# Kernel optimization log

Measured on AMD Instinct MI355X. Metric: run time of the kernel, lower is better.

The kernel has to match this reference:

```python
import jax, jax.numpy as jnp
from jax import lax
import numpy as np

EPS = 1e-6
DN = ('NCHW', 'OIHW', 'NCHW')  # conv dimension numbers matching torch F.conv2d


def setup_inputs() -> dict:
    key = jax.random.key(0)
    kx, ky = jax.random.split(key)
    B, C, H, W = 16, 3, 512, 512
    x = jax.random.normal(kx, (B, C, H, W), dtype=jnp.float32)
    y = jax.random.normal(ky, (B, C, H, W), dtype=jnp.float32)
    return {"x": x, "y": y}


def _box_smooth(v):
    # 7x7 uniform kernel repeated over 3 input channels -> 1 output channel,
    # every tap weighted 1/49 (matches kernel.repeat(1,3,1,1) in torch).
    k = jnp.full((1, v.shape[1], 7, 7), 1.0 / 49.0, dtype=v.dtype)
    return lax.conv_general_dilated(v, k, window_strides=(1, 1),
                                    padding=[(3, 3), (3, 3)],
                                    dimension_numbers=DN)


def reference(x, y):
    # conv is linear, so conv(x) - conv(y) == conv(x - y); avoids one conv pass
    diff = _box_smooth(x - y)           # [B, 1, H, W]
    return jnp.mean(jnp.sqrt(diff * diff + EPS))  # scalar Charbonnier loss
```

## Files before the change

### kernel.cpp

```cpp
#include <hip/hip_runtime.h>
#include <math.h>


namespace {
constexpr int kB = 16, kC = 3, kH = 512, kW = 512;
constexpr int ROWS = 2;
constexpr int INROWS = ROWS + 6;
constexpr int BANDS_PER_IMG = kH / ROWS;
constexpr int NBANDS = kB * BANDS_PER_IMG;
constexpr int WPB = 4;
constexpr int NT = WPB * 64;
constexpr int NB = NBANDS / WPB;
constexpr int NXCD = 8;
constexpr float EPS = 1e-6f;
}

struct RowRegs { float4 a[6]; float4 b[6]; };

__device__ __forceinline__ void issue_row(RowRegs& R,
                                          const float* __restrict__ xb,
                                          const float* __restrict__ yb,
                                          int rclamp, int c0) {
  const size_t HW = (size_t)kH * kW;
  const float* px = xb + (size_t)rclamp * kW + c0;
  const float* py = yb + (size_t)rclamp * kW + c0;
#pragma unroll
  for (int ch = 0; ch < 3; ++ch) {
    R.a[ch]     = *(const float4*)(px + ch * HW);
    R.b[ch]     = *(const float4*)(px + ch * HW + 4);
    R.a[3 + ch] = *(const float4*)(py + ch * HW);
    R.b[3 + ch] = *(const float4*)(py + ch * HW + 4);
  }
}

__global__ __launch_bounds__(NT, 1)
void charbox_kernel(const float* __restrict__ x, const float* __restrict__ y,
                    float* __restrict__ out) {
  __shared__ float red[WPB];

  const int tid  = threadIdx.x;
  const int lane = tid & 63;
  const int wid  = tid >> 6;
  const int swz  = (blockIdx.x % NXCD) * (NB / NXCD) + blockIdx.x / NXCD;
  const int band = swz * WPB + wid;
  const int b    = band >> 8;
  const int r0   = (band & 255) * ROWS;
  const size_t HW = (size_t)kH * kW;
  const float* xb = x + (size_t)b * kC * HW;
  const float* yb = y + (size_t)b * kC * HW;
  const int c0 = lane * 8;
  const int laneL = (lane + 63) & 63;
  const int laneR = (lane + 1) & 63;

  float v0[8], v1[8];
#pragma unroll
  for (int j = 0; j < 8; ++j) { v0[j] = 0.f; v1[j] = 0.f; }
  float acc = 0.f;

  RowRegs buf[2];
  issue_row(buf[0], xb, yb, max(r0 - 3, 0), c0);

#pragma unroll
  for (int it = 0; it < INROWS; ++it) {
    if (it + 1 < INROWS) {
      const int rn = r0 - 3 + it + 1;
      issue_row(buf[(it + 1) & 1], xb, yb, min(max(rn, 0), kH - 1), c0);
    }
    const RowRegs& R = buf[it & 1];
    const int r = r0 - 3 + it;
    const bool valid = (r >= 0) & (r < kH);

    float z[8];
    if (valid) {
      z[0] = (R.a[0].x - R.a[3].x) + (R.a[1].x - R.a[4].x) + (R.a[2].x - R.a[5].x);
      z[1] = (R.a[0].y - R.a[3].y) + (R.a[1].y - R.a[4].y) + (R.a[2].y - R.a[5].y);
      z[2] = (R.a[0].z - R.a[3].z) + (R.a[1].z - R.a[4].z) + (R.a[2].z - R.a[5].z);
      z[3] = (R.a[0].w - R.a[3].w) + (R.a[1].w - R.a[4].w) + (R.a[2].w - R.a[5].w);
      z[4] = (R.b[0].x - R.b[3].x) + (R.b[1].x - R.b[4].x) + (R.b[2].x - R.b[5].x);
      z[5] = (R.b[0].y - R.b[3].y) + (R.b[1].y - R.b[4].y) + (R.b[2].y - R.b[5].y);
      z[6] = (R.b[0].z - R.b[3].z) + (R.b[1].z - R.b[4].z) + (R.b[2].z - R.b[5].z);
      z[7] = (R.b[0].w - R.b[3].w) + (R.b[1].w - R.b[4].w) + (R.b[2].w - R.b[5].w);
    } else {
#pragma unroll
      for (int j = 0; j < 8; ++j) z[j] = 0.f;
    }

    const float l5 = __shfl(z[5], laneL, 64);
    const float l6 = __shfl(z[6], laneL, 64);
    const float l7 = __shfl(z[7], laneL, 64);
    const float g0 = __shfl(z[0], laneR, 64);
    const float g1 = __shfl(z[1], laneR, 64);
    const float g2 = __shfl(z[2], laneR, 64);
    float e[14];
    e[0] = lane ? l5 : 0.f;
    e[1] = lane ? l6 : 0.f;
    e[2] = lane ? l7 : 0.f;
#pragma unroll
    for (int j = 0; j < 8; ++j) e[3 + j] = z[j];
    e[11] = (lane < 63) ? g0 : 0.f;
    e[12] = (lane < 63) ? g1 : 0.f;
    e[13] = (lane < 63) ? g2 : 0.f;

    float h[8];
    float s = ((e[0] + e[1]) + (e[2] + e[3])) + ((e[4] + e[5]) + e[6]);
    h[0] = s;
#pragma unroll
    for (int j = 1; j < 8; ++j) {
      s += e[j + 6] - e[j - 1];
      h[j] = s;
    }

    if (it <= 6) {
#pragma unroll
      for (int j = 0; j < 8; ++j) v0[j] += h[j];
    }
    if (it >= 1) {
#pragma unroll
      for (int j = 0; j < 8; ++j) v1[j] += h[j];
    }
  }

#pragma unroll
  for (int j = 0; j < 8; ++j) {
    const float d0 = v0[j] * (1.0f / 49.0f);
    acc += sqrtf(fmaf(d0, d0, EPS));
    const float d1 = v1[j] * (1.0f / 49.0f);
    acc += sqrtf(fmaf(d1, d1, EPS));
  }

#pragma unroll
  for (int off = 32; off > 0; off >>= 1) acc += __shfl_down(acc, off, 64);
  if (lane == 0) red[wid] = acc;
  __syncthreads();
  if (tid == 0) {
    const float ssum = (red[0] + red[1]) + (red[2] + red[3]);
    atomicAdd(out, ssum * (1.0f / ((float)kB * (float)kH * (float)kW)));
  }
}

extern "C" void kernel_launch(void* const* d_in, const int* in_sizes, int n_in,
                              void* d_out, int out_size, void* d_ws, size_t ws_size,
                              hipStream_t stream) {
  const float* x = (const float*)d_in[0];
  const float* y = (const float*)d_in[1];
  float* out = (float*)d_out;

  charbox_kernel<<<NB, NT, 0, stream>>>(x, y, out);
}
```

Measured before the change: 127.3 us.

## Split into channel-diff precompute pass and box-filter pass over workspace

Adds a first kernel that reduces x-y over the three channels into a single-plane workspace, then a second kernel runs the 7x7 box filter on that plane with a three-deep row prefetch. This avoids re-reading all six input planes for every halo row (the old band of 2 rows read 8 rows of 6 planes). The cost is an extra workspace write and read of one plane plus a second launch. The fused kernel is kept as a fallback when the workspace is too small.

```diff
diff --git a/kernel.cpp b/kernel.cpp
--- a/kernel.cpp
+++ b/kernel.cpp
@@ -4,50 +4,67 @@
 
 namespace {
 constexpr int kB = 16, kC = 3, kH = 512, kW = 512;
+constexpr size_t HW = (size_t)kH * kW;
+constexpr size_t NPIX = (size_t)kB * HW;
+constexpr size_t Z_BYTES = NPIX * sizeof(float);
+constexpr float EPS = 1e-6f;
+constexpr int NXCD = 8;
+
+constexpr int P1_NT = 256;
+constexpr int P1_NB = (int)(NPIX / 4 / P1_NT);
+
 constexpr int ROWS = 2;
 constexpr int INROWS = ROWS + 6;
 constexpr int BANDS_PER_IMG = kH / ROWS;
 constexpr int NBANDS = kB * BANDS_PER_IMG;
 constexpr int WPB = 4;
-constexpr int NT = WPB * 64;
-constexpr int NB = NBANDS / WPB;
-constexpr int NXCD = 8;
-constexpr float EPS = 1e-6f;
-}
-
-struct RowRegs { float4 a[6]; float4 b[6]; };
-
-__device__ __forceinline__ void issue_row(RowRegs& R,
-                                          const float* __restrict__ xb,
-                                          const float* __restrict__ yb,
-                                          int rclamp, int c0) {
-  const size_t HW = (size_t)kH * kW;
-  const float* px = xb + (size_t)rclamp * kW + c0;
-  const float* py = yb + (size_t)rclamp * kW + c0;
-#pragma unroll
-  for (int ch = 0; ch < 3; ++ch) {
-    R.a[ch]     = *(const float4*)(px + ch * HW);
-    R.b[ch]     = *(const float4*)(px + ch * HW + 4);
-    R.a[3 + ch] = *(const float4*)(py + ch * HW);
-    R.b[3 + ch] = *(const float4*)(py + ch * HW + 4);
-  }
-}
-
-__global__ __launch_bounds__(NT, 1)
-void charbox_kernel(const float* __restrict__ x, const float* __restrict__ y,
-                    float* __restrict__ out) {
+constexpr int NT2 = WPB * 64;
+constexpr int NB2 = NBANDS / WPB;
+}
+
+__global__ __launch_bounds__(P1_NT)
+void zdiff_kernel(const float* __restrict__ x, const float* __restrict__ y,
+                  float* __restrict__ z) {
+  const int swz = (blockIdx.x % NXCD) * (P1_NB / NXCD) + blockIdx.x / NXCD;
+  const size_t i = (size_t)swz * P1_NT + threadIdx.x;
+  const size_t b = i >> 16;
+  const size_t p = (i & 65535) << 2;
+  const float* xb = x + b * kC * HW + p;
+  const float* yb = y + b * kC * HW + p;
+  const float4 x0 = *(const float4*)xb;
+  const float4 x1 = *(const float4*)(xb + HW);
+  const float4 x2 = *(const float4*)(xb + 2 * HW);
+  const float4 y0 = *(const float4*)yb;
+  const float4 y1 = *(const float4*)(yb + HW);
+  const float4 y2 = *(const float4*)(yb + 2 * HW);
+  float4 zz;
+  zz.x = (x0.x - y0.x) + (x1.x - y1.x) + (x2.x - y2.x);
+  zz.y = (x0.y - y0.y) + (x1.y - y1.y) + (x2.y - y2.y);
+  zz.z = (x0.z - y0.z) + (x1.z - y1.z) + (x2.z - y2.z);
+  zz.w = (x0.w - y0.w) + (x1.w - y1.w) + (x2.w - y2.w);
+  *(float4*)(z + b * HW + p) = zz;
+}
+
+struct ZRow { float4 a, b; };
+
+__device__ __forceinline__ void issue_zrow(ZRow& R, const float* __restrict__ zb,
+                                           int rclamp, int c0) {
+  const float* p = zb + (size_t)rclamp * kW + c0;
+  R.a = *(const float4*)p;
+  R.b = *(const float4*)(p + 4);
+}
+
+__global__ __launch_bounds__(NT2)
+void box_kernel(const float* __restrict__ z, float* __restrict__ out) {
   __shared__ float red[WPB];
-
   const int tid  = threadIdx.x;
   const int lane = tid & 63;
   const int wid  = tid >> 6;
-  const int swz  = (blockIdx.x % NXCD) * (NB / NXCD) + blockIdx.x / NXCD;
+  const int swz  = (blockIdx.x % NXCD) * (NB2 / NXCD) + blockIdx.x / NXCD;
   const int band = swz * WPB + wid;
   const int b    = band >> 8;
   const int r0   = (band & 255) * ROWS;
-  const size_t HW = (size_t)kH * kW;
-  const float* xb = x + (size_t)b * kC * HW;
-  const float* yb = y + (size_t)b * kC * HW;
+  const float* zb = z + (size_t)b * HW;
   const int c0 = lane * 8;
   const int laneL = (lane + 63) & 63;
   const int laneR = (lane + 1) & 63;
@@ -57,46 +74,41 @@
   for (int j = 0; j < 8; ++j) { v0[j] = 0.f; v1[j] = 0.f; }
   float acc = 0.f;
 
-  RowRegs buf[2];
-  issue_row(buf[0], xb, yb, max(r0 - 3, 0), c0);
+  ZRow buf[3];
+  issue_zrow(buf[0], zb, max(r0 - 3, 0), c0);
+  issue_zrow(buf[1], zb, min(max(r0 - 2, 0), kH - 1), c0);
 
 #pragma unroll
   for (int it = 0; it < INROWS; ++it) {
-    if (it + 1 < INROWS) {
-      const int rn = r0 - 3 + it + 1;
-      issue_row(buf[(it + 1) & 1], xb, yb, min(max(rn, 0), kH - 1), c0);
-    }
-    const RowRegs& R = buf[it & 1];
+    if (it + 2 < INROWS) {
+      const int rn = r0 - 3 + it + 2;
+      issue_zrow(buf[(it + 2) % 3], zb, min(max(rn, 0), kH - 1), c0);
+    }
+    const ZRow& R = buf[it % 3];
     const int r = r0 - 3 + it;
     const bool valid = (r >= 0) & (r < kH);
 
-    float z[8];
+    float zv[8];
     if (valid) {
-      z[0] = (R.a[0].x - R.a[3].x) + (R.a[1].x - R.a[4].x) + (R.a[2].x - R.a[5].x);
-      z[1] = (R.a[0].y - R.a[3].y) + (R.a[1].y - R.a[4].y) + (R.a[2].y - R.a[5].y);
-      z[2] = (R.a[0].z - R.a[3].z) + (R.a[1].z - R.a[4].z) + (R.a[2].z - R.a[5].z);
-      z[3] = (R.a[0].w - R.a[3].w) + (R.a[1].w - R.a[4].w) + (R.a[2].w - R.a[5].w);
-      z[4] = (R.b[0].x - R.b[3].x) + (R.b[1].x - R.b[4].x) + (R.b[2].x - R.b[5].x);
-      z[5] = (R.b[0].y - R.b[3].y) + (R.b[1].y - R.b[4].y) + (R.b[2].y - R.b[5].y);
-      z[6] = (R.b[0].z - R.b[3].z) + (R.b[1].z - R.b[4].z) + (R.b[2].z - R.b[5].z);
-      z[7] = (R.b[0].w - R.b[3].w) + (R.b[1].w - R.b[4].w) + (R.b[2].w - R.b[5].w);
+      zv[0] = R.a.x; zv[1] = R.a.y; zv[2] = R.a.z; zv[3] = R.a.w;
+      zv[4] = R.b.x; zv[5] = R.b.y; zv[6] = R.b.z; zv[7] = R.b.w;
     } else {
 #pragma unroll
-      for (int j = 0; j < 8; ++j) z[j] = 0.f;
-    }
-
-    const float l5 = __shfl(z[5], laneL, 64);
-    const float l6 = __shfl(z[6], laneL, 64);
-    const float l7 = __shfl(z[7], laneL, 64);
-    const float g0 = __shfl(z[0], laneR, 64);
-    const float g1 = __shfl(z[1], laneR, 64);
-    const float g2 = __shfl(z[2], laneR, 64);
+      for (int j = 0; j < 8; ++j) zv[j] = 0.f;
+    }
+
+    const float l5 = __shfl(zv[5], laneL, 64);
+    const float l6 = __shfl(zv[6], laneL, 64);
+    const float l7 = __shfl(zv[7], laneL, 64);
+    const float g0 = __shfl(zv[0], laneR, 64);
+    const float g1 = __shfl(zv[1], laneR, 64);
+    const float g2 = __shfl(zv[2], laneR, 64);
     float e[14];
     e[0] = lane ? l5 : 0.f;
     e[1] = lane ? l6 : 0.f;
     e[2] = lane ? l7 : 0.f;
 #pragma unroll
-    for (int j = 0; j < 8; ++j) e[3 + j] = z[j];
+    for (int j = 0; j < 8; ++j) e[3 + j] = zv[j];
     e[11] = (lane < 63) ? g0 : 0.f;
     e[12] = (lane < 63) ? g1 : 0.f;
     e[13] = (lane < 63) ? g2 : 0.f;
@@ -138,6 +150,125 @@
   }
 }
 
+struct RowRegs { float4 a[6]; float4 b[6]; };
+
+__device__ __forceinline__ void issue_row(RowRegs& R,
+                                          const float* __restrict__ xb,
+                                          const float* __restrict__ yb,
+                                          int rclamp, int c0) {
+  const float* px = xb + (size_t)rclamp * kW + c0;
+  const float* py = yb + (size_t)rclamp * kW + c0;
+#pragma unroll
+  for (int ch = 0; ch < 3; ++ch) {
+    R.a[ch]     = *(const float4*)(px + ch * HW);
+    R.b[ch]     = *(const float4*)(px + ch * HW + 4);
+    R.a[3 + ch] = *(const float4*)(py + ch * HW);
+    R.b[3 + ch] = *(const float4*)(py + ch * HW + 4);
+  }
+}
+
+__global__ __launch_bounds__(NT2, 1)
+void charbox_fallback(const float* __restrict__ x, const float* __restrict__ y,
+                      float* __restrict__ out) {
+  __shared__ float red[WPB];
+  const int tid  = threadIdx.x;
+  const int lane = tid & 63;
+  const int wid  = tid >> 6;
+  const int swz  = (blockIdx.x % NXCD) * (NB2 / NXCD) + blockIdx.x / NXCD;
+  const int band = swz * WPB + wid;
+  const int b    = band >> 8;
+  const int r0   = (band & 255) * ROWS;
+  const float* xb = x + (size_t)b * kC * HW;
+  const float* yb = y + (size_t)b * kC * HW;
+  const int c0 = lane * 8;
+  const int laneL = (lane + 63) & 63;
+  const int laneR = (lane + 1) & 63;
+
+  float v0[8], v1[8];
+#pragma unroll
+  for (int j = 0; j < 8; ++j) { v0[j] = 0.f; v1[j] = 0.f; }
+  float acc = 0.f;
+
+  RowRegs buf[2];
+  issue_row(buf[0], xb, yb, max(r0 - 3, 0), c0);
+
+#pragma unroll
+  for (int it = 0; it < INROWS; ++it) {
+    if (it + 1 < INROWS) {
+      const int rn = r0 - 3 + it + 1;
+      issue_row(buf[(it + 1) & 1], xb, yb, min(max(rn, 0), kH - 1), c0);
+    }
+    const RowRegs& R = buf[it & 1];
+    const int r = r0 - 3 + it;
+    const bool valid = (r >= 0) & (r < kH);
+
+    float zv[8];
+    if (valid) {
+      zv[0] = (R.a[0].x - R.a[3].x) + (R.a[1].x - R.a[4].x) + (R.a[2].x - R.a[5].x);
+      zv[1] = (R.a[0].y - R.a[3].y) + (R.a[1].y - R.a[4].y) + (R.a[2].y - R.a[5].y);
+      zv[2] = (R.a[0].z - R.a[3].z) + (R.a[1].z - R.a[4].z) + (R.a[2].z - R.a[5].z);
+      zv[3] = (R.a[0].w - R.a[3].w) + (R.a[1].w - R.a[4].w) + (R.a[2].w - R.a[5].w);
+      zv[4] = (R.b[0].x - R.b[3].x) + (R.b[1].x - R.b[4].x) + (R.b[2].x - R.b[5].x);
+      zv[5] = (R.b[0].y - R.b[3].y) + (R.b[1].y - R.b[4].y) + (R.b[2].y - R.b[5].y);
+      zv[6] = (R.b[0].z - R.b[3].z) + (R.b[1].z - R.b[4].z) + (R.b[2].z - R.b[5].z);
+      zv[7] = (R.b[0].w - R.b[3].w) + (R.b[1].w - R.b[4].w) + (R.b[2].w - R.b[5].w);
+    } else {
+#pragma unroll
+      for (int j = 0; j < 8; ++j) zv[j] = 0.f;
+    }
+
+    const float l5 = __shfl(zv[5], laneL, 64);
+    const float l6 = __shfl(zv[6], laneL, 64);
+    const float l7 = __shfl(zv[7], laneL, 64);
+    const float g0 = __shfl(zv[0], laneR, 64);
+    const float g1 = __shfl(zv[1], laneR, 64);
+    const float g2 = __shfl(zv[2], laneR, 64);
+    float e[14];
+    e[0] = lane ? l5 : 0.f;
+    e[1] = lane ? l6 : 0.f;
+    e[2] = lane ? l7 : 0.f;
+#pragma unroll
+    for (int j = 0; j < 8; ++j) e[3 + j] = zv[j];
+    e[11] = (lane < 63) ? g0 : 0.f;
+    e[12] = (lane < 63) ? g1 : 0.f;
+    e[13] = (lane < 63) ? g2 : 0.f;
+
+    float h[8];
+    float s = ((e[0] + e[1]) + (e[2] + e[3])) + ((e[4] + e[5]) + e[6]);
+    h[0] = s;
+#pragma unroll
+    for (int j = 1; j < 8; ++j) {
+      s += e[j + 6] - e[j - 1];
+      h[j] = s;
+    }
+    if (it <= 6) {
+#pragma unroll
+      for (int j = 0; j < 8; ++j) v0[j] += h[j];
+    }
+    if (it >= 1) {
+#pragma unroll
+      for (int j = 0; j < 8; ++j) v1[j] += h[j];
+    }
+  }
+
+#pragma unroll
+  for (int j = 0; j < 8; ++j) {
+    const float d0 = v0[j] * (1.0f / 49.0f);
+    acc += sqrtf(fmaf(d0, d0, EPS));
+    const float d1 = v1[j] * (1.0f / 49.0f);
+    acc += sqrtf(fmaf(d1, d1, EPS));
+  }
+
+#pragma unroll
+  for (int off = 32; off > 0; off >>= 1) acc += __shfl_down(acc, off, 64);
+  if (lane == 0) red[wid] = acc;
+  __syncthreads();
+  if (tid == 0) {
+    const float ssum = (red[0] + red[1]) + (red[2] + red[3]);
+    atomicAdd(out, ssum * (1.0f / ((float)kB * (float)kH * (float)kW)));
+  }
+}
+
 extern "C" void kernel_launch(void* const* d_in, const int* in_sizes, int n_in,
                               void* d_out, int out_size, void* d_ws, size_t ws_size,
                               hipStream_t stream) {
@@ -145,5 +276,11 @@
   const float* y = (const float*)d_in[1];
   float* out = (float*)d_out;
 
-  charbox_kernel<<<NB, NT, 0, stream>>>(x, y, out);
-}
+  if (ws_size >= Z_BYTES) {
+    float* zws = (float*)d_ws;
+    zdiff_kernel<<<P1_NB, P1_NT, 0, stream>>>(x, y, zws);
+    box_kernel<<<NB2, NT2, 0, stream>>>(zws, out);
+  } else {
+    charbox_fallback<<<NB2, NT2, 0, stream>>>(x, y, out);
+  }
+}
```

After: 132.5 us. 1.04x slower.
